# Optimization experiments

Measured on AMD Instinct MI355X. Metric: run time of the kernel, lower is better.

## Reference

```python
import jax, jax.numpy as jnp
import numpy as np

B = 256   # number of segments
P = 2000  # points per segment (hard-coded by fc_1 = Linear(2000*32, 1024))
C = 32    # point feature channels
EPS_BN = 1e-5


def _bn_relu(h, g, b):
    # BatchNorm1d in training mode: batch statistics over axis 0, biased variance.
    m = jnp.mean(h, axis=0)
    v = jnp.var(h, axis=0)
    return jax.nn.relu((h - m) * jax.lax.rsqrt(v + EPS_BN) * g + b)


def setup_inputs() -> dict:
    key = jax.random.key(0)
    ks = jax.random.split(key, 16)
    s = 0.02
    inp = {
        "x": jax.random.normal(ks[0], (B * P, C), jnp.float32),
        "length": jnp.full((B,), P, dtype=jnp.int32),
        # attention MLP (1x1 conv1d chain 32->16->8->1), torch layout [out,in]
        "w1": jax.random.normal(ks[1], (16, 32), jnp.float32) * s,
        "b1": jnp.zeros((16,), jnp.float32),
        "g1": jnp.ones((16,), jnp.float32),
        "be1": jnp.zeros((16,), jnp.float32),
        "w2": jax.random.normal(ks[2], (8, 16), jnp.float32) * s,
        "b2": jnp.zeros((8,), jnp.float32),
        "g2": jnp.ones((8,), jnp.float32),
        "be2": jnp.zeros((8,), jnp.float32),
        "w3": jax.random.normal(ks[3], (1, 8), jnp.float32) * s,
        "b3": jnp.zeros((1,), jnp.float32),
        "g3": jnp.ones((1,), jnp.float32),
        "be3": jnp.zeros((1,), jnp.float32),
        # FC head
        "fw1": jax.random.normal(ks[4], (1024, P * C), jnp.float32) * s,
        "fb1": jnp.zeros((1024,), jnp.float32),
        "fg1": jnp.ones((1024,), jnp.float32),
        "fbe1": jnp.zeros((1024,), jnp.float32),
        "fw2": jax.random.normal(ks[5], (256, 1024), jnp.float32) * s,
        "fb2": jnp.zeros((256,), jnp.float32),
        "fg2": jnp.ones((256,), jnp.float32),
        "fbe2": jnp.zeros((256,), jnp.float32),
    }
    return inp


def reference(x, length, w1, b1, g1, be1, w2, b2, g2, be2, w3, b3, g3, be3,
              fw1, fb1, fg1, fbe1, fw2, fb2, fg2, fbe2):
    # Pointwise attention score MLP over all points (BN stats over the full
    # point dimension, matching conv1d+BatchNorm1d with batch size 1).
    h = _bn_relu(x @ w1.T + b1, g1, be1)          # [N,16]
    h = _bn_relu(h @ w2.T + b2, g2, be2)          # [N,8]
    score = _bn_relu(h @ w3.T + b3, g3, be3)      # [N,1]

    # Per-segment softmax over the point dim, then weighted features + flatten.
    # All segments have exactly P=2000 points (required by fc_1's input dim),
    # so the ragged slicing collapses to a dense [B,P,*] reshape.
    att = jax.nn.softmax(score.reshape(B, P, 1), axis=1)   # [B,P,1]
    pooled = (x.reshape(B, P, C) * att).reshape(B, P * C)  # [B,64000]

    r = _bn_relu(pooled @ fw1.T + fb1, fg1, fbe1)  # [B,1024]
    r = _bn_relu(r @ fw2.T + fb2, fg2, fbe2)       # [B,256]

    # F.normalize(p=2, dim=1, eps=1e-12)
    norm = jnp.maximum(jnp.linalg.norm(r, axis=1, keepdims=True), 1e-12)
    return r / norm
```

## Files before the change

kernel.cpp:

```cpp
#include <hip/hip_runtime.h>
#include <hip/hip_bf16.h>

#define NPTS   512000
#define BSEG   256
#define PSEG   2000
#define CIN    32
#define INV_N  (1.0f/512000.0f)
#define EPS_BN 1e-5f

#define S1_OFF 0
#define S2_OFF 1024
#define S3_OFF 1536
#define S4_OFF 1600
#define S5_OFF 9792

using u32 = unsigned int;
using u16 = unsigned short;
using f32x4  = __attribute__((ext_vector_type(4))) float;
using bf16x8 = __attribute__((ext_vector_type(8))) short;

static __device__ __forceinline__ u16 f2bf(float f) {
    u32 u = __builtin_bit_cast(u32, f);
    u += 0x7fffu + ((u >> 16) & 1u);
    return (u16)(u >> 16);
}

static __device__ __forceinline__ void gload_lds16(const void* g, void* l) {
    __builtin_amdgcn_global_load_lds(
        (const __attribute__((address_space(1))) unsigned int*)g,
        (__attribute__((address_space(3))) unsigned int*)l, 16, 0, 0);
}

__global__ __launch_bounds__(256) void k_zero(float4* __restrict__ p) {
    p[blockIdx.x * 256 + threadIdx.x] = float4{0.0f, 0.0f, 0.0f, 0.0f};
}

__global__ __launch_bounds__(256) void k_mlp1(const float* __restrict__ x,
                                              const float* __restrict__ w1,
                                              float* __restrict__ a1,
                                              float* __restrict__ stats) {
    __shared__ float w[512];
    __shared__ float part[4][32];
    const int t = threadIdx.x;
    w[t] = w1[t]; w[t + 256] = w1[t + 256];
    __syncthreads();

    const int idx = blockIdx.x * 256 + t;
    const float4* xr = (const float4*)(x + (size_t)idx * 32);
    float4 xv[8];
#pragma unroll
    for (int i = 0; i < 8; i++) xv[i] = xr[i];

    float h[16];
#pragma unroll
    for (int c = 0; c < 16; c++) {
        float s = 0.0f;
        const float4* wr = (const float4*)(w + c * 32);
#pragma unroll
        for (int i = 0; i < 8; i++) {
            float4 wv = wr[i];
            s += xv[i].x * wv.x + xv[i].y * wv.y + xv[i].z * wv.z + xv[i].w * wv.w;
        }
        h[c] = s;
    }

    float4* ar = (float4*)(a1 + (size_t)idx * 16);
#pragma unroll
    for (int i = 0; i < 4; i++) {
        float4 o; o.x = h[i*4+0]; o.y = h[i*4+1]; o.z = h[i*4+2]; o.w = h[i*4+3];
        ar[i] = o;
    }

    const int lane = t & 63, wave = t >> 6;
#pragma unroll
    for (int c = 0; c < 16; c++) {
        float s = h[c], q = h[c] * h[c];
#pragma unroll
        for (int off = 32; off > 0; off >>= 1) {
            s += __shfl_down(s, off);
            q += __shfl_down(q, off);
        }
        if (lane == 0) { part[wave][c] = s; part[wave][16 + c] = q; }
    }
    __syncthreads();
    if (t < 32) {
        float tot = part[0][t] + part[1][t] + part[2][t] + part[3][t];
        atomicAdd(&stats[S1_OFF + (blockIdx.x & 31) * 32 + t], tot);
    }
}

__global__ __launch_bounds__(256) void k_mlp2(const float* __restrict__ a1,
                                              const float* __restrict__ w2,
                                              const float* __restrict__ g1,
                                              const float* __restrict__ be1,
                                              float* __restrict__ a2,
                                              float* __restrict__ stats) {
    __shared__ float w[128];
    __shared__ float sc[16], sh[16];
    __shared__ float part[4][16];
    const int t = threadIdx.x;
    if (t < 128) w[t] = w2[t];
    if (t < 16) {
        float s = 0.0f, q = 0.0f;
#pragma unroll 8
        for (int c = 0; c < 32; c++) {
            s += stats[S1_OFF + c * 32 + t];
            q += stats[S1_OFF + c * 32 + 16 + t];
        }
        float m = s * INV_N;
        float v = q * INV_N - m * m;
        float sl = g1[t] * rsqrtf(v + EPS_BN);
        sc[t] = sl; sh[t] = be1[t] - m * sl;
    }
    __syncthreads();

    const int idx = blockIdx.x * 256 + t;
    const float4* ar = (const float4*)(a1 + (size_t)idx * 16);
    float h[16];
#pragma unroll
    for (int i = 0; i < 4; i++) {
        float4 v4 = ar[i];
        h[i*4+0] = v4.x; h[i*4+1] = v4.y; h[i*4+2] = v4.z; h[i*4+3] = v4.w;
    }
#pragma unroll
    for (int c = 0; c < 16; c++) h[c] = fmaxf(fmaf(h[c], sc[c], sh[c]), 0.0f);

    float o[8];
#pragma unroll
    for (int c = 0; c < 8; c++) {
        float s = 0.0f;
#pragma unroll
        for (int k = 0; k < 16; k++) s += h[k] * w[c * 16 + k];
        o[c] = s;
    }
    float4* orp = (float4*)(a2 + (size_t)idx * 8);
    float4 o0; o0.x=o[0]; o0.y=o[1]; o0.z=o[2]; o0.w=o[3];
    float4 o1; o1.x=o[4]; o1.y=o[5]; o1.z=o[6]; o1.w=o[7];
    orp[0] = o0; orp[1] = o1;

    const int lane = t & 63, wave = t >> 6;
#pragma unroll
    for (int c = 0; c < 8; c++) {
        float s = o[c], q = o[c] * o[c];
#pragma unroll
        for (int off = 32; off > 0; off >>= 1) {
            s += __shfl_down(s, off);
            q += __shfl_down(q, off);
        }
        if (lane == 0) { part[wave][c] = s; part[wave][8 + c] = q; }
    }
    __syncthreads();
    if (t < 16) {
        float tot = part[0][t] + part[1][t] + part[2][t] + part[3][t];
        atomicAdd(&stats[S2_OFF + (blockIdx.x & 31) * 16 + t], tot);
    }
}

__global__ __launch_bounds__(256) void k_mlp3(const float* __restrict__ a2,
                                              const float* __restrict__ w3,
                                              const float* __restrict__ g2,
                                              const float* __restrict__ be2,
                                              float* __restrict__ a3,
                                              float* __restrict__ stats) {
    __shared__ float w[8], sc[8], sh[8];
    __shared__ float part[4][2];
    const int t = threadIdx.x;
    if (t < 8) {
        w[t] = w3[t];
        float s = 0.0f, q = 0.0f;
#pragma unroll 8
        for (int c = 0; c < 32; c++) {
            s += stats[S2_OFF + c * 16 + t];
            q += stats[S2_OFF + c * 16 + 8 + t];
        }
        float m = s * INV_N;
        float v = q * INV_N - m * m;
        float sl = g2[t] * rsqrtf(v + EPS_BN);
        sc[t] = sl; sh[t] = be2[t] - m * sl;
    }
    __syncthreads();

    const int idx = blockIdx.x * 256 + t;
    const float4* ar = (const float4*)(a2 + (size_t)idx * 8);
    float4 v0 = ar[0], v1 = ar[1];
    float h[8] = {v0.x, v0.y, v0.z, v0.w, v1.x, v1.y, v1.z, v1.w};
    float s = 0.0f;
#pragma unroll
    for (int c = 0; c < 8; c++) s += fmaxf(fmaf(h[c], sc[c], sh[c]), 0.0f) * w[c];
    a3[idx] = s;

    const int lane = t & 63, wave = t >> 6;
    float q = s * s;
    float ss = s;
#pragma unroll
    for (int off = 32; off > 0; off >>= 1) {
        ss += __shfl_down(ss, off);
        q  += __shfl_down(q, off);
    }
    if (lane == 0) { part[wave][0] = ss; part[wave][1] = q; }
    __syncthreads();
    if (t < 2) {
        float tot = part[0][t] + part[1][t] + part[2][t] + part[3][t];
        atomicAdd(&stats[S3_OFF + (blockIdx.x & 31) * 2 + t], tot);
    }
}

__global__ __launch_bounds__(256) void k_pool(const float* __restrict__ a3,
                                              const float* __restrict__ x,
                                              const float* __restrict__ g3,
                                              const float* __restrict__ be3,
                                              const float* __restrict__ stats,
                                              u16* __restrict__ pooled) {
    const int b = blockIdx.x, t = threadIdx.x;
    float sm = 0.0f, sq = 0.0f;
#pragma unroll 8
    for (int c = 0; c < 32; c++) {
        sm += stats[S3_OFF + c * 2];
        sq += stats[S3_OFF + c * 2 + 1];
    }
    const float m  = sm * INV_N;
    const float v  = sq * INV_N - m * m;
    const float sc = g3[0] * rsqrtf(v + EPS_BN);
    const float sh = be3[0] - m * sc;

    float sv[8];
    float mx = -1e30f;
#pragma unroll
    for (int i = 0; i < 8; i++) {
        int p = t + i * 256;
        if (p < PSEG) {
            float val = fmaxf(fmaf(a3[(size_t)b * PSEG + p], sc, sh), 0.0f);
            sv[i] = val; mx = fmaxf(mx, val);
        } else sv[i] = -1e30f;
    }
    const int lane = t & 63, wave = t >> 6;
    __shared__ float redm[4], reds[4];
#pragma unroll
    for (int off = 32; off > 0; off >>= 1) mx = fmaxf(mx, __shfl_xor(mx, off));
    if (lane == 0) redm[wave] = mx;
    __syncthreads();
    mx = fmaxf(fmaxf(redm[0], redm[1]), fmaxf(redm[2], redm[3]));

    float es = 0.0f;
#pragma unroll
    for (int i = 0; i < 8; i++) {
        int p = t + i * 256;
        if (p < PSEG) { float e = __expf(sv[i] - mx); sv[i] = e; es += e; }
    }
#pragma unroll
    for (int off = 32; off > 0; off >>= 1) es += __shfl_xor(es, off);
    if (lane == 0) reds[wave] = es;
    __syncthreads();
    const float inv = 1.0f / (reds[0] + reds[1] + reds[2] + reds[3]);

    const int swz = (b & 7) << 3;
#pragma unroll
    for (int i = 0; i < 8; i++) {
        int p = t + i * 256;
        if (p >= PSEG) continue;
        const float att = sv[i] * inv;
        const float4* xr = (const float4*)(x + ((size_t)b * PSEG + p) * 32);
        u16* dst = pooled + (size_t)b * 64000 + (size_t)(p >> 1) * 64;
        const int half = (p & 1) << 5;
#pragma unroll
        for (int u = 0; u < 4; u++) {
            float4 f0 = xr[u * 2], f1 = xr[u * 2 + 1];
            u32 q0 = (u32)f2bf(f0.x * att) | ((u32)f2bf(f0.y * att) << 16);
            u32 q1 = (u32)f2bf(f0.z * att) | ((u32)f2bf(f0.w * att) << 16);
            u32 q2 = (u32)f2bf(f1.x * att) | ((u32)f2bf(f1.y * att) << 16);
            u32 q3 = (u32)f2bf(f1.z * att) | ((u32)f2bf(f1.w * att) << 16);
            uint4 q; q.x = q0; q.y = q1; q.z = q2; q.w = q3;
            *(uint4*)(dst + ((half | (u << 3)) ^ swz)) = q;
        }
    }
}

__global__ __launch_bounds__(256) void k_gemm4(const u16* __restrict__ pooled,
                                               const float* __restrict__ fw1,
                                               float* __restrict__ a4p) {
    __shared__ alignas(16) char smem[40960];
    char* As = smem;
    char* Bs = smem + 32768;

    const int t = threadIdx.x;
    const int jblk = blockIdx.x;
    const int kblk = blockIdx.y;
    const int wave = t >> 6, lane = t & 63;
    const int kbase = kblk * 1600;

    f32x4 acc[4][4] = {};

    for (int step = 0; step < 25; ++step) {
        const int k0 = kbase + step * 64;
        {
            const u16* gs = pooled + (size_t)(wave * 8 + (lane >> 3)) * 64000
                            + k0 + (lane & 7) * 8;
            char* ld = As + wave * 1024;
#pragma unroll
            for (int i = 0; i < 8; i++)
                gload_lds16(gs + (size_t)i * 32 * 64000, ld + i * 4096);
        }
        {
            const int jj = t >> 4;
            const int ks = (t & 15) * 4;
#pragma unroll
            for (int i = 0; i < 4; i++) {
                const int j = i * 16 + jj;
                float4 v = *(const float4*)(fw1 + (size_t)(jblk * 64 + j) * 64000 + k0 + ks);
                ushort4 bv;
                bv.x = f2bf(v.x); bv.y = f2bf(v.y); bv.z = f2bf(v.z); bv.w = f2bf(v.w);
                const int byte = (j * 128 + ks * 2) ^ ((j & 7) << 4);
                *(ushort4*)(Bs + byte) = bv;
            }
        }
        __syncthreads();
#pragma unroll
        for (int kk = 0; kk < 2; ++kk) {
            const int krow = kk * 32 + (lane >> 4) * 8;
            bf16x8 aF[4], bF[4];
#pragma unroll
            for (int mm = 0; mm < 4; mm++) {
                const int row = wave * 64 + mm * 16 + (lane & 15);
                aF[mm] = *(const bf16x8*)(As + ((row * 128 + krow * 2) ^ ((row & 7) << 4)));
            }
#pragma unroll
            for (int nn = 0; nn < 4; nn++) {
                const int col = nn * 16 + (lane & 15);
                bF[nn] = *(const bf16x8*)(Bs + ((col * 128 + krow * 2) ^ ((col & 7) << 4)));
            }
#pragma unroll
            for (int mm = 0; mm < 4; mm++)
#pragma unroll
                for (int nn = 0; nn < 4; nn++)
                    acc[mm][nn] = __builtin_amdgcn_mfma_f32_16x16x32_bf16(
                        aF[mm], bF[nn], acc[mm][nn], 0, 0, 0);
        }
        __syncthreads();
    }

    float* dst = a4p + (size_t)kblk * 262144;
#pragma unroll
    for (int mm = 0; mm < 4; mm++)
#pragma unroll
        for (int nn = 0; nn < 4; nn++)
#pragma unroll
            for (int r = 0; r < 4; r++) {
                const int row = wave * 64 + mm * 16 + (lane >> 4) * 4 + r;
                const int col = jblk * 64 + nn * 16 + (lane & 15);
                dst[(size_t)row * 1024 + col] = acc[mm][nn][r];
            }
}

__global__ __launch_bounds__(256) void k_red4(const float* __restrict__ a4p,
                                              float* __restrict__ a4,
                                              float* __restrict__ stats) {
    const int i = blockIdx.x, t = threadIdx.x;
    float4 s = {0.0f, 0.0f, 0.0f, 0.0f};
#pragma unroll 8
    for (int kb = 0; kb < 40; kb++) {
        float4 v = *(const float4*)(a4p + (size_t)kb * 262144 + (size_t)i * 1024 + t * 4);
        s.x += v.x; s.y += v.y; s.z += v.z; s.w += v.w;
    }
    *(float4*)(a4 + (size_t)i * 1024 + t * 4) = s;
    const int j = t * 4;
    float* s4 = stats + S4_OFF + (i & 3) * 2048;
    atomicAdd(&s4[j + 0], s.x);
    atomicAdd(&s4[j + 1], s.y);
    atomicAdd(&s4[j + 2], s.z);
    atomicAdd(&s4[j + 3], s.w);
    atomicAdd(&s4[1024 + j + 0], s.x * s.x);
    atomicAdd(&s4[1024 + j + 1], s.y * s.y);
    atomicAdd(&s4[1024 + j + 2], s.z * s.z);
    atomicAdd(&s4[1024 + j + 3], s.w * s.w);
}

__global__ __launch_bounds__(256) void k_fc2(const float* __restrict__ a4,
                                             const float* __restrict__ fg1,
                                             const float* __restrict__ fbe1,
                                             const float* __restrict__ fw2,
                                             float* __restrict__ stats,
                                             float* __restrict__ a5) {
    __shared__ alignas(16) float h[1024];
    const int i = blockIdx.x, t = threadIdx.x;
#pragma unroll
    for (int u = 0; u < 4; u++) {
        const int k = u * 256 + t;
        float s = 0.0f, q = 0.0f;
#pragma unroll
        for (int c = 0; c < 4; c++) {
            s += stats[S4_OFF + c * 2048 + k];
            q += stats[S4_OFF + c * 2048 + 1024 + k];
        }
        float m  = s * (1.0f / 256.0f);
        float v  = q * (1.0f / 256.0f) - m * m;
        float sc = fg1[k] * rsqrtf(v + EPS_BN);
        float sh = fbe1[k] - m * sc;
        h[k] = fmaxf(fmaf(a4[(size_t)i * 1024 + k], sc, sh), 0.0f);
    }
    __syncthreads();
    const float4* wr = (const float4*)(fw2 + (size_t)t * 1024);
    const float4* hr = (const float4*)h;
    float s = 0.0f;
#pragma unroll 4
    for (int u = 0; u < 256; u++) {
        float4 w = wr[u], hv = hr[u];
        s += w.x * hv.x + w.y * hv.y + w.z * hv.z + w.w * hv.w;
    }
    a5[(size_t)i * 256 + t] = s;
    float* s5 = stats + S5_OFF + (i & 15) * 512;
    atomicAdd(&s5[t], s);
    atomicAdd(&s5[256 + t], s * s);
}

__global__ __launch_bounds__(256) void k_norm(const float* __restrict__ a5,
                                              const float* __restrict__ fg2,
                                              const float* __restrict__ fbe2,
                                              const float* __restrict__ stats,
                                              float* __restrict__ out) {
    const int i = blockIdx.x, t = threadIdx.x;
    float s = 0.0f, q2 = 0.0f;
#pragma unroll
    for (int c = 0; c < 16; c++) {
        s  += stats[S5_OFF + c * 512 + t];
        q2 += stats[S5_OFF + c * 512 + 256 + t];
    }
    float m  = s * (1.0f / 256.0f);
    float v  = q2 * (1.0f / 256.0f) - m * m;
    float sc = fg2[t] * rsqrtf(v + EPS_BN);
    float sh = fbe2[t] - m * sc;
    float r = fmaxf(fmaf(a5[(size_t)i * 256 + t], sc, sh), 0.0f);

    float q = r * r;
    const int lane = t & 63, wave = t >> 6;
#pragma unroll
    for (int off = 32; off > 0; off >>= 1) q += __shfl_xor(q, off);
    __shared__ float red[4];
    if (lane == 0) red[wave] = q;
    __syncthreads();
    float tot = red[0] + red[1] + red[2] + red[3];
    float nrm = fmaxf(sqrtf(tot), 1e-12f);
    out[(size_t)i * 256 + t] = r / nrm;
}

extern "C" void kernel_launch(void* const* d_in, const int* in_sizes, int n_in,
                              void* d_out, int out_size, void* d_ws, size_t ws_size,
                              hipStream_t stream) {
    const float* x   = (const float*)d_in[0];
    const float* w1  = (const float*)d_in[2];
    const float* g1  = (const float*)d_in[4];
    const float* be1 = (const float*)d_in[5];
    const float* w2  = (const float*)d_in[6];
    const float* g2  = (const float*)d_in[8];
    const float* be2 = (const float*)d_in[9];
    const float* w3  = (const float*)d_in[10];
    const float* g3  = (const float*)d_in[12];
    const float* be3 = (const float*)d_in[13];
    const float* fw1 = (const float*)d_in[14];
    const float* fg1 = (const float*)d_in[16];
    const float* fbe1= (const float*)d_in[17];
    const float* fw2 = (const float*)d_in[18];
    const float* fg2 = (const float*)d_in[20];
    const float* fbe2= (const float*)d_in[21];
    float* out = (float*)d_out;

    char* ws = (char*)d_ws;
    float* stats = (float*)ws;
    float* a4 = (float*)(ws + 73728);
    float* a5 = (float*)(ws + 73728 + 1048576);
    float* a4p = (float*)(ws + 73728 + 1048576 + 262144);
    char*  big = ws + 73728 + 1048576 + 262144 + 41943040;
    float* a1 = (float*)big;
    u16*   pooled = (u16*)big;
    float* a2 = (float*)(big + 32768000);
    float* a3 = (float*)(big + 32768000 + 16384000);

    k_zero<<<18, 256, 0, stream>>>((float4*)ws);
    k_mlp1<<<2000, 256, 0, stream>>>(x, w1, a1, stats);
    k_mlp2<<<2000, 256, 0, stream>>>(a1, w2, g1, be1, a2, stats);
    k_mlp3<<<2000, 256, 0, stream>>>(a2, w3, g2, be2, a3, stats);
    k_pool<<<256, 256, 0, stream>>>(a3, x, g3, be3, stats, pooled);
    k_gemm4<<<dim3(16, 40), 256, 0, stream>>>(pooled, fw1, a4p);
    k_red4<<<256, 256, 0, stream>>>(a4p, a4, stats);
    k_fc2<<<256, 256, 0, stream>>>(a4, fg1, fbe1, fw2, stats, a5);
    k_norm<<<256, 256, 0, stream>>>(a5, fg2, fbe2, stats, out);
}
```

Measured before the change: 276.4 us.

## Double-buffer LDS tiles in fc1 GEMM to overlap loads with MFMA

Turns the k_gemm4 main loop into a two-stage pipeline. Shared memory grows to two A/B tile buffers, and the next step's pooled tile (async global-to-LDS loads) and fw1 tile (register prefetch) are issued before the current step's MFMAs. The prefetched fw1 values are converted to bf16 and stored after compute, which cuts the loop to one barrier per step. In exchange, LDS use doubles to 80KB, which limits blocks per CU, and register pressure rises from holding the prefetched float4s.

```diff
diff --git a/kernel.cpp b/kernel.cpp
--- a/kernel.cpp
+++ b/kernel.cpp
@@ -2,9 +2,7 @@
 #include <hip/hip_bf16.h>
 
 #define NPTS   512000
-#define BSEG   256
 #define PSEG   2000
-#define CIN    32
 #define INV_N  (1.0f/512000.0f)
 #define EPS_BN 1e-5f
 
@@ -278,9 +276,7 @@
 __global__ __launch_bounds__(256) void k_gemm4(const u16* __restrict__ pooled,
                                                const float* __restrict__ fw1,
                                                float* __restrict__ a4p) {
-    __shared__ alignas(16) char smem[40960];
-    char* As = smem;
-    char* Bs = smem + 32768;
+    __shared__ alignas(16) char smem[81920];
 
     const int t = threadIdx.x;
     const int jblk = blockIdx.x;
@@ -288,32 +284,53 @@
     const int wave = t >> 6, lane = t & 63;
     const int kbase = kblk * 1600;
 
+    const u16* gA = pooled + (size_t)(wave * 8 + (lane >> 3)) * 64000 + (lane & 7) * 8;
+    const int jj = t >> 4;
+    const int ks = (t & 15) * 4;
+
     f32x4 acc[4][4] = {};
-
+    float4 bn0, bn1, bn2, bn3;
+
+    {
+#pragma unroll
+        for (int i = 0; i < 8; i++)
+            gload_lds16(gA + kbase + (size_t)i * 32 * 64000,
+                        smem + wave * 1024 + i * 4096);
+        const float* bsrc = fw1 + (size_t)(jblk * 64 + jj) * 64000 + kbase + ks;
+        bn0 = *(const float4*)(bsrc);
+        bn1 = *(const float4*)(bsrc + (size_t)16 * 64000);
+        bn2 = *(const float4*)(bsrc + (size_t)32 * 64000);
+        bn3 = *(const float4*)(bsrc + (size_t)48 * 64000);
+        char* Bs = smem + 32768;
+#pragma unroll
+        for (int i = 0; i < 4; i++) {
+            const int j = i * 16 + jj;
+            float4 v = (i == 0) ? bn0 : (i == 1) ? bn1 : (i == 2) ? bn2 : bn3;
+            ushort4 bv;
+            bv.x = f2bf(v.x); bv.y = f2bf(v.y); bv.z = f2bf(v.z); bv.w = f2bf(v.w);
+            *(ushort4*)(Bs + ((j * 128 + ks * 2) ^ ((j & 7) << 4))) = bv;
+        }
+    }
+    __syncthreads();
+
+    int curoff = 0;
     for (int step = 0; step < 25; ++step) {
-        const int k0 = kbase + step * 64;
-        {
-            const u16* gs = pooled + (size_t)(wave * 8 + (lane >> 3)) * 64000
-                            + k0 + (lane & 7) * 8;
-            char* ld = As + wave * 1024;
+        const int nxtoff = curoff ^ 40960;
+        const bool pf = (step + 1 < 25);
+        if (pf) {
+            const int k1 = kbase + (step + 1) * 64;
+            const float* bsrc = fw1 + (size_t)(jblk * 64 + jj) * 64000 + k1 + ks;
+            bn0 = *(const float4*)(bsrc);
+            bn1 = *(const float4*)(bsrc + (size_t)16 * 64000);
+            bn2 = *(const float4*)(bsrc + (size_t)32 * 64000);
+            bn3 = *(const float4*)(bsrc + (size_t)48 * 64000);
 #pragma unroll
             for (int i = 0; i < 8; i++)
-                gload_lds16(gs + (size_t)i * 32 * 64000, ld + i * 4096);
-        }
-        {
-            const int jj = t >> 4;
-            const int ks = (t & 15) * 4;
-#pragma unroll
-            for (int i = 0; i < 4; i++) {
-                const int j = i * 16 + jj;
-                float4 v = *(const float4*)(fw1 + (size_t)(jblk * 64 + j) * 64000 + k0 + ks);
-                ushort4 bv;
-                bv.x = f2bf(v.x); bv.y = f2bf(v.y); bv.z = f2bf(v.z); bv.w = f2bf(v.w);
-                const int byte = (j * 128 + ks * 2) ^ ((j & 7) << 4);
-                *(ushort4*)(Bs + byte) = bv;
-            }
-        }
-        __syncthreads();
+                gload_lds16(gA + k1 + (size_t)i * 32 * 64000,
+                            smem + nxtoff + wave * 1024 + i * 4096);
+        }
+        const char* As = smem + curoff;
+        const char* Bs = smem + curoff + 32768;
 #pragma unroll
         for (int kk = 0; kk < 2; ++kk) {
             const int krow = kk * 32 + (lane >> 4) * 8;
@@ -335,7 +352,19 @@
                     acc[mm][nn] = __builtin_amdgcn_mfma_f32_16x16x32_bf16(
                         aF[mm], bF[nn], acc[mm][nn], 0, 0, 0);
         }
+        if (pf) {
+            char* Bn = smem + nxtoff + 32768;
+#pragma unroll
+            for (int i = 0; i < 4; i++) {
+                const int j = i * 16 + jj;
+                float4 v = (i == 0) ? bn0 : (i == 1) ? bn1 : (i == 2) ? bn2 : bn3;
+                ushort4 bv;
+                bv.x = f2bf(v.x); bv.y = f2bf(v.y); bv.z = f2bf(v.z); bv.w = f2bf(v.w);
+                *(ushort4*)(Bn + ((j * 128 + ks * 2) ^ ((j & 7) << 4))) = bv;
+            }
+        }
         __syncthreads();
+        curoff = nxtoff;
     }
 
     float* dst = a4p + (size_t)kblk * 262144;
```

Result: no change. 274.0 us (-0.9%).

## Software-pipeline fc1 GEMM with register-resident A fragments and double-buffered B tile

Applied to the files above, without the earlier changes.

The pooled activation layout is changed to plain row-major so each lane can load its A-operand MFMA fragments straight from global memory into registers, which removes the A tile from LDS. The B (fw1) tile is double-buffered in LDS, and the next step's global loads are issued before the current step's MFMAs, with explicit waitcnt and barriers so loads overlap compute. Workgroup IDs are also remapped so that blocks sharing the same k-slice are grouped together, which may improve L2 reuse. The cost is higher register pressure and uncoalesced strided 16-byte A loads, and the hand-written waitcnt values are fragile.

```diff
diff --git a/kernel.cpp b/kernel.cpp
--- a/kernel.cpp
+++ b/kernel.cpp
@@ -2,9 +2,7 @@
 #include <hip/hip_bf16.h>
 
 #define NPTS   512000
-#define BSEG   256
 #define PSEG   2000
-#define CIN    32
 #define INV_N  (1.0f/512000.0f)
 #define EPS_BN 1e-5f
 
@@ -23,12 +21,6 @@
     u32 u = __builtin_bit_cast(u32, f);
     u += 0x7fffu + ((u >> 16) & 1u);
     return (u16)(u >> 16);
-}
-
-static __device__ __forceinline__ void gload_lds16(const void* g, void* l) {
-    __builtin_amdgcn_global_load_lds(
-        (const __attribute__((address_space(1))) unsigned int*)g,
-        (__attribute__((address_space(3))) unsigned int*)l, 16, 0, 0);
 }
 
 __global__ __launch_bounds__(256) void k_zero(float4* __restrict__ p) {
@@ -253,15 +245,13 @@
     __syncthreads();
     const float inv = 1.0f / (reds[0] + reds[1] + reds[2] + reds[3]);
 
-    const int swz = (b & 7) << 3;
 #pragma unroll
     for (int i = 0; i < 8; i++) {
         int p = t + i * 256;
         if (p >= PSEG) continue;
         const float att = sv[i] * inv;
         const float4* xr = (const float4*)(x + ((size_t)b * PSEG + p) * 32);
-        u16* dst = pooled + (size_t)b * 64000 + (size_t)(p >> 1) * 64;
-        const int half = (p & 1) << 5;
+        u16* dst = pooled + (size_t)b * 64000 + (size_t)p * 32;
 #pragma unroll
         for (int u = 0; u < 4; u++) {
             float4 f0 = xr[u * 2], f1 = xr[u * 2 + 1];
@@ -270,7 +260,7 @@
             u32 q2 = (u32)f2bf(f1.x * att) | ((u32)f2bf(f1.y * att) << 16);
             u32 q3 = (u32)f2bf(f1.z * att) | ((u32)f2bf(f1.w * att) << 16);
             uint4 q; q.x = q0; q.y = q1; q.z = q2; q.w = q3;
-            *(uint4*)(dst + ((half | (u << 3)) ^ swz)) = q;
+            *(uint4*)(dst + u * 8) = q;
         }
     }
 }
@@ -278,65 +268,108 @@
 __global__ __launch_bounds__(256) void k_gemm4(const u16* __restrict__ pooled,
                                                const float* __restrict__ fw1,
                                                float* __restrict__ a4p) {
-    __shared__ alignas(16) char smem[40960];
-    char* As = smem;
-    char* Bs = smem + 32768;
+    __shared__ alignas(16) char Bs[16384];
 
     const int t = threadIdx.x;
-    const int jblk = blockIdx.x;
-    const int kblk = blockIdx.y;
+    const int wgid = blockIdx.y * 16 + blockIdx.x;
+    const int xr = wgid & 7, qq = wgid >> 3;
+    const int jblk = qq & 15;
+    const int kblk = xr + ((qq >> 4) << 3);
     const int wave = t >> 6, lane = t & 63;
     const int kbase = kblk * 1600;
 
+    const u16* gA = pooled + (size_t)(wave * 64 + (lane & 15)) * 64000
+                    + (lane >> 4) * 8 + kbase;
+    const int jj = t >> 4, ks = (t & 15) * 4;
+    const float* gB = fw1 + (size_t)(jblk * 64 + jj) * 64000 + ks + kbase;
+
     f32x4 acc[4][4] = {};
-
-    for (int step = 0; step < 25; ++step) {
-        const int k0 = kbase + step * 64;
-        {
-            const u16* gs = pooled + (size_t)(wave * 8 + (lane >> 3)) * 64000
-                            + k0 + (lane & 7) * 8;
-            char* ld = As + wave * 1024;
-#pragma unroll
-            for (int i = 0; i < 8; i++)
-                gload_lds16(gs + (size_t)i * 32 * 64000, ld + i * 4096);
-        }
-        {
-            const int jj = t >> 4;
-            const int ks = (t & 15) * 4;
-#pragma unroll
-            for (int i = 0; i < 4; i++) {
-                const int j = i * 16 + jj;
-                float4 v = *(const float4*)(fw1 + (size_t)(jblk * 64 + j) * 64000 + k0 + ks);
-                ushort4 bv;
-                bv.x = f2bf(v.x); bv.y = f2bf(v.y); bv.z = f2bf(v.z); bv.w = f2bf(v.w);
-                const int byte = (j * 128 + ks * 2) ^ ((j & 7) << 4);
-                *(ushort4*)(Bs + byte) = bv;
-            }
-        }
-        __syncthreads();
-#pragma unroll
-        for (int kk = 0; kk < 2; ++kk) {
-            const int krow = kk * 32 + (lane >> 4) * 8;
-            bf16x8 aF[4], bF[4];
-#pragma unroll
-            for (int mm = 0; mm < 4; mm++) {
-                const int row = wave * 64 + mm * 16 + (lane & 15);
-                aF[mm] = *(const bf16x8*)(As + ((row * 128 + krow * 2) ^ ((row & 7) << 4)));
-            }
-#pragma unroll
-            for (int nn = 0; nn < 4; nn++) {
-                const int col = nn * 16 + (lane & 15);
-                bF[nn] = *(const bf16x8*)(Bs + ((col * 128 + krow * 2) ^ ((col & 7) << 4)));
-            }
-#pragma unroll
-            for (int mm = 0; mm < 4; mm++)
-#pragma unroll
-                for (int nn = 0; nn < 4; nn++)
-                    acc[mm][nn] = __builtin_amdgcn_mfma_f32_16x16x32_bf16(
-                        aF[mm], bF[nn], acc[mm][nn], 0, 0, 0);
-        }
-        __syncthreads();
-    }
+    bf16x8 aA[8], aB[8];
+    float4 b0, b1, b2, b3;
+
+#pragma unroll
+    for (int mm = 0; mm < 4; mm++)
+#pragma unroll
+        for (int kk = 0; kk < 2; kk++)
+            aA[mm * 2 + kk] = *(const bf16x8*)(gA + (size_t)mm * 16 * 64000 + kk * 32);
+    b0 = *(const float4*)(gB);
+    b1 = *(const float4*)(gB + (size_t)16 * 64000);
+    b2 = *(const float4*)(gB + (size_t)32 * 64000);
+    b3 = *(const float4*)(gB + (size_t)48 * 64000);
+#pragma unroll
+    for (int i = 0; i < 4; i++) {
+        const int j = i * 16 + jj;
+        float4 v = (i == 0) ? b0 : (i == 1) ? b1 : (i == 2) ? b2 : b3;
+        ushort4 bv;
+        bv.x = f2bf(v.x); bv.y = f2bf(v.y); bv.z = f2bf(v.z); bv.w = f2bf(v.w);
+        *(ushort4*)(Bs + ((j * 128 + ks * 2) ^ ((j & 7) << 4))) = bv;
+    }
+    __syncthreads();
+
+#define GSTEP(ACUR, ANXT, STEP, CUROFF)                                         \
+    {                                                                           \
+        const bool pf = (STEP) < 24;                                            \
+        if (pf) {                                                               \
+            const float* bs = gB + ((STEP) + 1) * 64;                           \
+            b0 = *(const float4*)(bs);                                          \
+            b1 = *(const float4*)(bs + (size_t)16 * 64000);                     \
+            b2 = *(const float4*)(bs + (size_t)32 * 64000);                     \
+            b3 = *(const float4*)(bs + (size_t)48 * 64000);                     \
+            const u16* as = gA + ((STEP) + 1) * 64;                             \
+            _Pragma("unroll")                                                   \
+            for (int mm = 0; mm < 4; mm++)                                      \
+                _Pragma("unroll")                                               \
+                for (int kk = 0; kk < 2; kk++)                                  \
+                    ANXT[mm * 2 + kk] = *(const bf16x8*)(                       \
+                        as + (size_t)mm * 16 * 64000 + kk * 32);                \
+        }                                                                       \
+        __builtin_amdgcn_sched_barrier(0);                                      \
+        _Pragma("unroll")                                                       \
+        for (int kk = 0; kk < 2; kk++) {                                        \
+            const int krow = kk * 32 + (lane >> 4) * 8;                         \
+            bf16x8 bF[4];                                                       \
+            _Pragma("unroll")                                                   \
+            for (int nn = 0; nn < 4; nn++) {                                    \
+                const int col = nn * 16 + (lane & 15);                          \
+                bF[nn] = *(const bf16x8*)(Bs + (CUROFF) +                       \
+                         ((col * 128 + krow * 2) ^ ((col & 7) << 4)));          \
+            }                                                                   \
+            _Pragma("unroll")                                                   \
+            for (int mm = 0; mm < 4; mm++)                                      \
+                _Pragma("unroll")                                               \
+                for (int nn = 0; nn < 4; nn++)                                  \
+                    acc[mm][nn] = __builtin_amdgcn_mfma_f32_16x16x32_bf16(      \
+                        ACUR[mm * 2 + kk], bF[nn], acc[mm][nn], 0, 0, 0);       \
+        }                                                                       \
+        __builtin_amdgcn_sched_barrier(0);                                      \
+        __builtin_amdgcn_s_barrier();                                           \
+        if (pf) {                                                               \
+            asm volatile("s_waitcnt vmcnt(8)" ::: "memory");                    \
+            __builtin_amdgcn_sched_barrier(0);                                  \
+            char* Bw = Bs + ((CUROFF) ^ 8192);                                  \
+            _Pragma("unroll")                                                   \
+            for (int i = 0; i < 4; i++) {                                       \
+                const int j = i * 16 + jj;                                      \
+                float4 v = (i == 0) ? b0 : (i == 1) ? b1 : (i == 2) ? b2 : b3;  \
+                ushort4 bv;                                                     \
+                bv.x = f2bf(v.x); bv.y = f2bf(v.y);                             \
+                bv.z = f2bf(v.z); bv.w = f2bf(v.w);                             \
+                *(ushort4*)(Bw + ((j * 128 + ks * 2) ^ ((j & 7) << 4))) = bv;   \
+            }                                                                   \
+            asm volatile("s_waitcnt lgkmcnt(0)" ::: "memory");                  \
+            __builtin_amdgcn_sched_barrier(0);                                  \
+            __builtin_amdgcn_s_barrier();                                       \
+        }                                                                       \
+    }
+
+#pragma unroll 1
+    for (int it = 0; it < 12; ++it) {
+        const int s0 = it * 2;
+        GSTEP(aA, aB, s0, 0);
+        GSTEP(aB, aA, s0 + 1, 8192);
+    }
+    GSTEP(aA, aB, 24, 0);
+#undef GSTEP
 
     float* dst = a4p + (size_t)kblk * 262144;
 #pragma unroll
```

After: 305.0 us. +10.3%, slower.

## Double-buffer LDS in fc1 GEMM with prefetch two steps ahead

Applied to the files above, without the earlier changes.

Rewrites the big fc_1 GEMM main loop to double-buffer the A (pooled) and B (fw1) tiles in LDS. Global loads for step+2 are issued while MFMAs run on the current buffer, and explicit vmcnt waits plus sched_barriers control the overlap. It also raises wave priority around the MFMA block. LDS usage doubles to 80KB, which may reduce occupancy, and the hand-written waitcnt counts must match the number of loads issued.

```diff
diff --git a/kernel.cpp b/kernel.cpp
--- a/kernel.cpp
+++ b/kernel.cpp
@@ -2,9 +2,7 @@
 #include <hip/hip_bf16.h>
 
 #define NPTS   512000
-#define BSEG   256
 #define PSEG   2000
-#define CIN    32
 #define INV_N  (1.0f/512000.0f)
 #define EPS_BN 1e-5f
 
@@ -278,9 +276,7 @@
 __global__ __launch_bounds__(256) void k_gemm4(const u16* __restrict__ pooled,
                                                const float* __restrict__ fw1,
                                                float* __restrict__ a4p) {
-    __shared__ alignas(16) char smem[40960];
-    char* As = smem;
-    char* Bs = smem + 32768;
+    __shared__ alignas(16) char smem[81920];
 
     const int t = threadIdx.x;
     const int jblk = blockIdx.x;
@@ -288,32 +284,57 @@
     const int wave = t >> 6, lane = t & 63;
     const int kbase = kblk * 1600;
 
+    const u16* gA = pooled + (size_t)(wave * 8 + (lane >> 3)) * 64000 + (lane & 7) * 8 + kbase;
+    const int jj = t >> 4;
+    const int ks = (t & 15) * 4;
+    const float* gB = fw1 + (size_t)(jblk * 64 + jj) * 64000 + ks + kbase;
+
     f32x4 acc[4][4] = {};
-
+    float4 b0, b1, b2, b3;
+
+#define ISSUE_B(STEP) {                                                       \
+        const float* bs = gB + (STEP) * 64;                                   \
+        b0 = *(const float4*)(bs);                                            \
+        b1 = *(const float4*)(bs + (size_t)16 * 64000);                       \
+        b2 = *(const float4*)(bs + (size_t)32 * 64000);                       \
+        b3 = *(const float4*)(bs + (size_t)48 * 64000); }
+#define ISSUE_A(STEP, BUF) {                                                  \
+        _Pragma("unroll")                                                     \
+        for (int i = 0; i < 8; i++)                                           \
+            gload_lds16(gA + (STEP) * 64 + (size_t)i * 32 * 64000,            \
+                        smem + (BUF) * 32768 + wave * 1024 + i * 4096); }
+#define WRITE_B(BUF) {                                                        \
+        char* Bw = smem + 65536 + (BUF) * 8192;                               \
+        _Pragma("unroll")                                                     \
+        for (int i = 0; i < 4; i++) {                                         \
+            const int j = i * 16 + jj;                                        \
+            float4 v = (i == 0) ? b0 : (i == 1) ? b1 : (i == 2) ? b2 : b3;    \
+            ushort4 bv;                                                       \
+            bv.x = f2bf(v.x); bv.y = f2bf(v.y);                               \
+            bv.z = f2bf(v.z); bv.w = f2bf(v.w);                               \
+            *(ushort4*)(Bw + ((j * 128 + ks * 2) ^ ((j & 7) << 4))) = bv; } }
+
+    ISSUE_B(0);
+    __builtin_amdgcn_sched_barrier(0);
+    ISSUE_A(0, 0);
+    __builtin_amdgcn_sched_barrier(0);
+    asm volatile("s_waitcnt vmcnt(8)" ::: "memory");
+    __builtin_amdgcn_sched_barrier(0);
+    WRITE_B(0);
+    ISSUE_B(1);
+    __builtin_amdgcn_sched_barrier(0);
+    ISSUE_A(1, 1);
+    __builtin_amdgcn_sched_barrier(0);
+    asm volatile("s_waitcnt vmcnt(12) lgkmcnt(0)" ::: "memory");
+    __builtin_amdgcn_sched_barrier(0);
+    __builtin_amdgcn_s_barrier();
+
+    int cur = 0;
+#pragma unroll 1
     for (int step = 0; step < 25; ++step) {
-        const int k0 = kbase + step * 64;
-        {
-            const u16* gs = pooled + (size_t)(wave * 8 + (lane >> 3)) * 64000
-                            + k0 + (lane & 7) * 8;
-            char* ld = As + wave * 1024;
-#pragma unroll
-            for (int i = 0; i < 8; i++)
-                gload_lds16(gs + (size_t)i * 32 * 64000, ld + i * 4096);
-        }
-        {
-            const int jj = t >> 4;
-            const int ks = (t & 15) * 4;
-#pragma unroll
-            for (int i = 0; i < 4; i++) {
-                const int j = i * 16 + jj;
-                float4 v = *(const float4*)(fw1 + (size_t)(jblk * 64 + j) * 64000 + k0 + ks);
-                ushort4 bv;
-                bv.x = f2bf(v.x); bv.y = f2bf(v.y); bv.z = f2bf(v.z); bv.w = f2bf(v.w);
-                const int byte = (j * 128 + ks * 2) ^ ((j & 7) << 4);
-                *(ushort4*)(Bs + byte) = bv;
-            }
-        }
-        __syncthreads();
+        const char* As = smem + cur * 32768;
+        const char* Bs = smem + 65536 + cur * 8192;
+        __builtin_amdgcn_s_setprio(1);
 #pragma unroll
         for (int kk = 0; kk < 2; ++kk) {
             const int krow = kk * 32 + (lane >> 4) * 8;
@@ -335,8 +356,33 @@
                     acc[mm][nn] = __builtin_amdgcn_mfma_f32_16x16x32_bf16(
                         aF[mm], bF[nn], acc[mm][nn], 0, 0, 0);
         }
-        __syncthreads();
-    }
+        __builtin_amdgcn_s_setprio(0);
+        __builtin_amdgcn_sched_barrier(0);
+        __builtin_amdgcn_s_barrier();
+        __builtin_amdgcn_sched_barrier(0);
+        if (step + 1 < 25) {
+            asm volatile("s_waitcnt vmcnt(8)" ::: "memory");
+            __builtin_amdgcn_sched_barrier(0);
+            WRITE_B(cur ^ 1);
+            __builtin_amdgcn_sched_barrier(0);
+            if (step + 2 < 25) {
+                ISSUE_B(step + 2);
+                __builtin_amdgcn_sched_barrier(0);
+                ISSUE_A(step + 2, cur);
+                __builtin_amdgcn_sched_barrier(0);
+                asm volatile("s_waitcnt vmcnt(12) lgkmcnt(0)" ::: "memory");
+            } else {
+                asm volatile("s_waitcnt vmcnt(0) lgkmcnt(0)" ::: "memory");
+            }
+            __builtin_amdgcn_sched_barrier(0);
+            __builtin_amdgcn_s_barrier();
+            __builtin_amdgcn_sched_barrier(0);
+        }
+        cur ^= 1;
+    }
+#undef ISSUE_B
+#undef ISSUE_A
+#undef WRITE_B
 
     float* dst = a4p + (size_t)kblk * 262144;
 #pragma unroll
```

Result: faster. 267.0 us (median of 2 runs) (-3.4%).
